# Kernel tuning notes

Hardware: AMD Instinct MI355X
Metric: run time of the kernel (lower is better)

The kernel has to match this reference:

```python
import jax, jax.numpy as jnp
import numpy as np

B, S, D = 4, 2048, 1024
P = 9            # num_paths
DM = D // 4      # bottleneck d_mid
EPS = 1e-5


def setup_inputs() -> dict:
    key = jax.random.key(0)
    ks = jax.random.split(key, 12)
    sc_in = 1.0 / np.sqrt(D)
    sc_mid = 1.0 / np.sqrt(DM)
    return {
        "x": jax.random.normal(ks[0], (B, S, D), dtype=jnp.float32),
        # neighbor mixer: per-channel 3-tap kernel over the sequence axis
        "mix_kernel": jax.random.normal(ks[1], (3, D), dtype=jnp.float32) * 0.5,
        # 9 parallel bottleneck paths: D -> D/4 -> D
        "W1": jax.random.normal(ks[2], (P, D, DM), dtype=jnp.float32) * sc_in,
        "b1": jnp.zeros((P, DM), dtype=jnp.float32),
        "W2": jax.random.normal(ks[3], (P, DM, D), dtype=jnp.float32) * sc_mid,
        "b2": jnp.zeros((P, D), dtype=jnp.float32),
        # observer: D -> D/4 -> tanh -> ... -> P scores
        "Wo1": jax.random.normal(ks[4], (D, DM), dtype=jnp.float32) * sc_in,
        "bo1": jnp.zeros((DM,), dtype=jnp.float32),
        "Wo2": jax.random.normal(ks[5], (DM, P), dtype=jnp.float32) * sc_mid,
        "bo2": jnp.zeros((P,), dtype=jnp.float32),
        # output norm affine params
        "gamma": jnp.ones((D,), dtype=jnp.float32),
        "beta": jnp.zeros((D,), dtype=jnp.float32),
    }


def _mix(x, mix_kernel):
    # eidosNeighborMixer: local 3-tap depthwise mix along sequence (non-causal)
    xp = jnp.pad(x, ((0, 0), (1, 1), (0, 0)))
    return (mix_kernel[0] * xp[:, :-2]
            + mix_kernel[1] * xp[:, 1:-1]
            + mix_kernel[2] * xp[:, 2:])


def _layernorm(h, gamma, beta):
    mu = jnp.mean(h, axis=-1, keepdims=True)
    var = jnp.var(h, axis=-1, keepdims=True)
    return (h - mu) * jax.lax.rsqrt(var + EPS) * gamma + beta


def reference(x, mix_kernel, W1, b1, W2, b2, Wo1, bo1, Wo2, bo2, gamma, beta):
    x_mixed = _mix(x, mix_kernel)                                   # [B,S,D]
    # all num_paths bottleneck transforms computed densely (as in source)
    h = jnp.einsum("bsd,pdm->bspm", x_mixed, W1) + b1               # [B,S,P,DM]
    stacked_paths = jnp.einsum("bspm,pmd->bspd", h, W2) + b2        # [B,S,P,D]
    # observer scores
    scores = jnp.tanh(x_mixed @ Wo1 + bo1) @ Wo2 + bo2              # [B,S,P]
    # eval-mode collapse: hard argmax one-hot selection
    idx = jnp.argmax(scores, axis=-1)                               # [B,S]
    weights = jax.nn.one_hot(idx, P, dtype=stacked_paths.dtype)     # [B,S,P]
    collapsed = jnp.einsum("bspd,bsp->bsd", stacked_paths, weights)  # [B,S,D]
    return _layernorm(x + collapsed, gamma, beta)
```

## Files before the change

### kernel.cpp

```cpp
#include <hip/hip_runtime.h>
#include <math.h>

#define Ss 2048
#define Dd 1024
#define Pp 9
#define DMm 256
#define Tt 8192
#define EPSf 1e-5f
#define BAND 6e-3f

typedef __attribute__((ext_vector_type(8))) __bf16 bf16x8;
typedef __attribute__((ext_vector_type(4))) float f32x4;

#define GLOBAL_AS __attribute__((address_space(1)))
#define LDS_AS __attribute__((address_space(3)))

#define MAXTILES 137

__device__ __forceinline__ unsigned short bf16rn(float f) {
  unsigned int u = __float_as_uint(f);
  unsigned int r = (u + 0x7fffu + ((u >> 16) & 1u)) >> 16;
  return (unsigned short)r;
}

__device__ __forceinline__ void gload16(const void* g, void* l) {
  __builtin_amdgcn_global_load_lds((const GLOBAL_AS unsigned int*)g,
                                   (LDS_AS unsigned int*)l, 16, 0, 0);
}

__device__ __forceinline__ int xcd_swz(int bx, int nwg) {
  const int q = nwg >> 3, r = nwg & 7;
  const int xcd = bx & 7, loc = bx >> 3;
  return (xcd < r ? xcd * (q + 1) : r * (q + 1) + (xcd - r) * q) + loc;
}

#define KSW(r, sl) (((r) << 6) + ((((sl) ^ ((r) & 7))) << 3))

__global__ __launch_bounds__(256) void k_mix2(const float* __restrict__ x,
    const float* __restrict__ mk, unsigned short* __restrict__ xh,
    int* __restrict__ counts) {
  if (blockIdx.x == 0 && threadIdx.x < 64) counts[threadIdx.x] = 0;
  const int t = xcd_swz(blockIdx.x, Tt);
  const int s = t & (Ss - 1);
  const int d = threadIdx.x << 2;
  const float* xc = x + (size_t)t * Dd + d;
  float4 vb = *(const float4*)xc;
  float4 va = make_float4(0.f, 0.f, 0.f, 0.f);
  float4 vc = make_float4(0.f, 0.f, 0.f, 0.f);
  if (s > 0)      va = *(const float4*)(xc - Dd);
  if (s < Ss - 1) vc = *(const float4*)(xc + Dd);
  const float4 k0 = *(const float4*)(mk + d);
  const float4 k1 = *(const float4*)(mk + Dd + d);
  const float4 k2 = *(const float4*)(mk + 2 * Dd + d);
  float4 o;
  o.x = k0.x * va.x + k1.x * vb.x + k2.x * vc.x;
  o.y = k0.y * va.y + k1.y * vb.y + k2.y * vc.y;
  o.z = k0.z * va.z + k1.z * vb.z + k2.z * vc.z;
  o.w = k0.w * va.w + k1.w * vb.w + k2.w * vc.w;
  ushort4 h;
  h.x = bf16rn(o.x); h.y = bf16rn(o.y); h.z = bf16rn(o.z); h.w = bf16rn(o.w);
  *(ushort4*)(xh + (size_t)t * Dd + d) = h;
}

__global__ __launch_bounds__(256) void k_cvt_all(
    const float* __restrict__ W1, const float* __restrict__ W2,
    const float* __restrict__ Wo1,
    unsigned short* __restrict__ W1t, unsigned short* __restrict__ W2t,
    unsigned short* __restrict__ Wo1t) {
  const int z = blockIdx.z;
  const float* in; unsigned short* outp; int R, C, r0, c0;
  if (z < Pp)            { in = W1;  outp = W1t;  R = Dd;  C = DMm;
                           r0 = blockIdx.x * 32; c0 = blockIdx.y * 32; }
  else if (z < 2 * Pp)   { in = W2;  outp = W2t;  R = DMm; C = Dd;
                           r0 = blockIdx.y * 32; c0 = blockIdx.x * 32; }
  else                   { in = Wo1; outp = Wo1t; R = Dd;  C = DMm;
                           r0 = blockIdx.x * 32; c0 = blockIdx.y * 32; }
  const int zi = (z < Pp) ? z : ((z < 2 * Pp) ? z - Pp : 0);
  const size_t zo = (size_t)zi * R * C;
  __shared__ float tile[32][33];
  const int tr = threadIdx.x >> 3, tc = (threadIdx.x & 7) << 2;
  float4 v = *(const float4*)(in + zo + (size_t)(r0 + tr) * C + c0 + tc);
  tile[tr][tc] = v.x; tile[tr][tc + 1] = v.y; tile[tr][tc + 2] = v.z; tile[tr][tc + 3] = v.w;
  __syncthreads();
  ushort4 h;
  h.x = bf16rn(tile[tc + 0][tr]); h.y = bf16rn(tile[tc + 1][tr]);
  h.z = bf16rn(tile[tc + 2][tr]); h.w = bf16rn(tile[tc + 3][tr]);
  *(ushort4*)(outp + zo + (size_t)(c0 + tr) * R + r0 + tc) = h;
}

template<int KTOT, int NTOT, int MODE, bool GROUPED>
__global__ __launch_bounds__(256) void k_gemm(
    const unsigned short* __restrict__ A,
    const unsigned short* __restrict__ Bt,
    const float* __restrict__ bias,
    const float* __restrict__ resid,
    float* __restrict__ outf, unsigned short* __restrict__ outh,
    const int* __restrict__ counts, const int* __restrict__ tokenlist) {
  int p = 0, ti = xcd_swz(blockIdx.x, gridDim.x), cnt = Tt;
  if (GROUPED) {
    for (p = 0; p < Pp; ++p) {
      cnt = counts[p];
      const int nt = (cnt + 63) >> 6;
      if (ti < nt) break;
      ti -= nt;
    }
    if (p == Pp) return;
  }
  const int tile0 = ti * 64;
  __shared__ int tl[64];
  __shared__ __align__(16) unsigned short As[2][64 * 64];
  __shared__ __align__(16) unsigned short Bs[2][128 * 64];
  const int tid = threadIdx.x;
  if (tid < 64) {
    const int li = tile0 + tid;
    if (GROUPED) tl[tid] = (li < cnt) ? tokenlist[p * Tt + li] : tokenlist[p * Tt];
    else         tl[tid] = li;
  }
  __syncthreads();
  const int w = tid >> 6, lane = tid & 63;
  const int fr = lane & 15, fs = lane >> 4;
  const int wr = w >> 1, wc = w & 1;
  const int n0 = blockIdx.y * 128;
  const unsigned short* Bp0 = Bt + (size_t)p * NTOT * KTOT + (size_t)n0 * KTOT;
  const unsigned short* srcA[2];
  #pragma unroll
  for (int i = 0; i < 2; ++i) {
    const int u = i * 256 + tid, r = u >> 3, sl = (u & 7) ^ (r & 7);
    srcA[i] = A + (size_t)tl[r] * KTOT + sl * 8;
  }
  const unsigned short* srcB[4];
  #pragma unroll
  for (int i = 0; i < 4; ++i) {
    const int u = i * 256 + tid, r = u >> 3, sl = (u & 7) ^ (r & 7);
    srcB[i] = Bp0 + (size_t)r * KTOT + sl * 8;
  }
  const int ldsW = w * 512;
  int aoff[2][2], boff[4][2];
  #pragma unroll
  for (int m = 0; m < 2; ++m)
    #pragma unroll
    for (int kk = 0; kk < 2; ++kk)
      aoff[m][kk] = KSW(wr * 32 + m * 16 + fr, kk * 4 + fs);
  #pragma unroll
  for (int n = 0; n < 4; ++n)
    #pragma unroll
    for (int kk = 0; kk < 2; ++kk)
      boff[n][kk] = KSW(wc * 64 + n * 16 + fr, kk * 4 + fs);

#define STAGE(b, kb) do { \
    gload16(srcA[0] + (kb), &As[b][0] + ldsW); \
    gload16(srcA[1] + (kb), &As[b][0] + 2048 + ldsW); \
    gload16(srcB[0] + (kb), &Bs[b][0] + ldsW); \
    gload16(srcB[1] + (kb), &Bs[b][0] + 2048 + ldsW); \
    gload16(srcB[2] + (kb), &Bs[b][0] + 4096 + ldsW); \
    gload16(srcB[3] + (kb), &Bs[b][0] + 6144 + ldsW); \
  } while (0)

  f32x4 acc[2][4] = {};
  const int NS = KTOT / 64;
  STAGE(0, 0);
  for (int s = 0; s < NS; ++s) {
    const int buf = s & 1;
    if (s + 1 < NS) {
      STAGE(buf ^ 1, (s + 1) * 64);
      asm volatile("s_waitcnt vmcnt(6)" ::: "memory");
    } else {
      asm volatile("s_waitcnt vmcnt(0)" ::: "memory");
    }
    __builtin_amdgcn_s_barrier();
    __builtin_amdgcn_sched_barrier(0);
    const unsigned short* Ab = &As[buf][0];
    const unsigned short* Bb_ = &Bs[buf][0];
    bf16x8 a[2][2], b[4][2];
    #pragma unroll
    for (int m = 0; m < 2; ++m)
      #pragma unroll
      for (int kk = 0; kk < 2; ++kk)
        a[m][kk] = *(const bf16x8*)&Ab[aoff[m][kk]];
    #pragma unroll
    for (int n = 0; n < 4; ++n)
      #pragma unroll
      for (int kk = 0; kk < 2; ++kk)
        b[n][kk] = *(const bf16x8*)&Bb_[boff[n][kk]];
    #pragma unroll
    for (int kk = 0; kk < 2; ++kk)
      #pragma unroll
      for (int m = 0; m < 2; ++m)
        #pragma unroll
        for (int n = 0; n < 4; ++n)
          acc[m][n] = __builtin_amdgcn_mfma_f32_16x16x32_bf16(a[m][kk], b[n][kk], acc[m][n], 0, 0, 0);
    __builtin_amdgcn_s_barrier();
  }
#undef STAGE

  const float* bias_z = bias + (size_t)p * NTOT;
  #pragma unroll
  for (int m = 0; m < 2; ++m) {
    #pragma unroll
    for (int j = 0; j < 4; ++j) {
      const int rr = wr * 32 + m * 16 + fs * 4 + j;
      const int li = tile0 + rr;
      if (GROUPED && li >= cnt) continue;
      const int t = tl[rr];
      #pragma unroll
      for (int n = 0; n < 4; ++n) {
        const int c = n0 + wc * 64 + n * 16 + fr;
        const float v = acc[m][n][j] + bias_z[c];
        if (MODE == 0)      outf[(size_t)t * NTOT + c] = tanhf(v);
        else if (MODE == 1) outh[(size_t)t * NTOT + c] = bf16rn(v);
        else                outf[(size_t)t * NTOT + c] = v + resid[(size_t)t * NTOT + c];
      }
    }
  }
}

__global__ __launch_bounds__(256) void k_score(const float* __restrict__ hidden,
    const float* __restrict__ Wo2, const float* __restrict__ bo2,
    int* __restrict__ idx, int* __restrict__ nflag, int* __restrict__ flagged) {
  __shared__ float sW[DMm * Pp];
  const int tid = threadIdx.x;
  for (int l = tid; l < DMm * Pp; l += 256) sW[l] = Wo2[l];
  __syncthreads();
  const int wave = tid >> 6, lane = tid & 63;
  const int t = blockIdx.x * 4 + wave;
  const float4 h = *(const float4*)(hidden + (size_t)t * DMm + lane * 4);
  const int m = lane * 4;
  float part[Pp];
  #pragma unroll
  for (int pp = 0; pp < Pp; ++pp)
    part[pp] = h.x * sW[(m + 0) * Pp + pp] + h.y * sW[(m + 1) * Pp + pp]
             + h.z * sW[(m + 2) * Pp + pp] + h.w * sW[(m + 3) * Pp + pp];
  #pragma unroll
  for (int off = 32; off > 0; off >>= 1)
    #pragma unroll
    for (int pp = 0; pp < Pp; ++pp)
      part[pp] += __shfl_xor(part[pp], off);
  if (lane == 0) {
    float best = -1e30f, second = -1e30f;
    int bi = 0;
    #pragma unroll
    for (int pp = 0; pp < Pp; ++pp) {
      const float sc = part[pp] + bo2[pp];
      if (sc > best) { second = best; best = sc; bi = pp; }
      else if (sc > second) second = sc;
    }
    idx[t] = bi;
    if (best - second < BAND) {
      const int pos = atomicAdd(nflag, 1);
      flagged[pos] = t;
    }
  }
}

__global__ __launch_bounds__(256) void k_rescue(const float* __restrict__ x,
    const float* __restrict__ mk,
    const float* __restrict__ Wo1, const float* __restrict__ bo1,
    const float* __restrict__ Wo2, const float* __restrict__ bo2,
    const int* __restrict__ nflag, const int* __restrict__ flagged,
    int* __restrict__ idx) {
  __shared__ double sx[Dd];
  __shared__ double th[DMm];
  __shared__ double red[4][12];
  const int nf = *nflag;
  const int tid = threadIdx.x;
  const int wv = tid >> 6, ln = tid & 63;
  for (int f = blockIdx.x; f < nf; f += gridDim.x) {
    const int t = flagged[f];
    const int s = t & (Ss - 1);
    for (int l = tid; l < Dd; l += 256) {
      const double xa = (s > 0)      ? (double)x[(size_t)(t - 1) * Dd + l] : 0.0;
      const double xb =                (double)x[(size_t)t * Dd + l];
      const double xc = (s < Ss - 1) ? (double)x[(size_t)(t + 1) * Dd + l] : 0.0;
      sx[l] = (double)mk[l] * xa + (double)mk[Dd + l] * xb + (double)mk[2 * Dd + l] * xc;
    }
    __syncthreads();
    {
      double a0 = 0, a1 = 0, a2 = 0, a3 = 0;
      const float* wcol = Wo1 + tid;
      for (int d = 0; d < Dd; d += 4) {
        a0 += sx[d + 0] * (double)wcol[(size_t)(d + 0) * DMm];
        a1 += sx[d + 1] * (double)wcol[(size_t)(d + 1) * DMm];
        a2 += sx[d + 2] * (double)wcol[(size_t)(d + 2) * DMm];
        a3 += sx[d + 3] * (double)wcol[(size_t)(d + 3) * DMm];
      }
      th[tid] = tanh(((a0 + a1) + (a2 + a3)) + (double)bo1[tid]);
    }
    __syncthreads();
    double pr[Pp];
    const double tv = th[tid];
    #pragma unroll
    for (int p = 0; p < Pp; ++p) pr[p] = tv * (double)Wo2[tid * Pp + p];
    #pragma unroll
    for (int off = 32; off > 0; off >>= 1)
      #pragma unroll
      for (int p = 0; p < Pp; ++p) pr[p] += __shfl_xor(pr[p], off);
    if (ln == 0) {
      #pragma unroll
      for (int p = 0; p < Pp; ++p) red[wv][p] = pr[p];
    }
    __syncthreads();
    if (tid == 0) {
      double best = -1e300; int bi = 0;
      #pragma unroll
      for (int p = 0; p < Pp; ++p) {
        const double sv = red[0][p] + red[1][p] + red[2][p] + red[3][p] + (double)bo2[p];
        if (sv > best) { best = sv; bi = p; }
      }
      idx[t] = bi;
    }
    __syncthreads();
  }
}

__global__ __launch_bounds__(256) void k_scatter(const int* __restrict__ idx,
    int* __restrict__ counts, int* __restrict__ tokenlist) {
  __shared__ int lcnt[Pp], lbase[Pp];
  const int tid = threadIdx.x;
  if (tid < Pp) lcnt[tid] = 0;
  __syncthreads();
  const int t = blockIdx.x * 256 + tid;
  const int p = idx[t];
  const int slot = atomicAdd(&lcnt[p], 1);
  __syncthreads();
  if (tid < Pp) lbase[tid] = atomicAdd(&counts[tid], lcnt[tid]);
  __syncthreads();
  tokenlist[p * Tt + lbase[p] + slot] = t;
}

__global__ __launch_bounds__(256) void k_ln(float* __restrict__ y,
    const float* __restrict__ gamma, const float* __restrict__ beta) {
  const int t = blockIdx.x;
  const int d = threadIdx.x << 2;
  float* row = y + (size_t)t * Dd;
  float4 v = *(float4*)(row + d);
  float s = v.x + v.y + v.z + v.w;
  float q = v.x * v.x + v.y * v.y + v.z * v.z + v.w * v.w;
  #pragma unroll
  for (int off = 32; off > 0; off >>= 1) {
    s += __shfl_xor(s, off);
    q += __shfl_xor(q, off);
  }
  __shared__ float ssum[4], sqq[4];
  const int wave = threadIdx.x >> 6, lane = threadIdx.x & 63;
  if (lane == 0) { ssum[wave] = s; sqq[wave] = q; }
  __syncthreads();
  s = ssum[0] + ssum[1] + ssum[2] + ssum[3];
  q = sqq[0] + sqq[1] + sqq[2] + sqq[3];
  const float mu = s * (1.f / Dd);
  const float var = q * (1.f / Dd) - mu * mu;
  const float inv = rsqrtf(var + EPSf);
  const float4 g = *(const float4*)(gamma + d);
  const float4 bt = *(const float4*)(beta + d);
  float4 o;
  o.x = (v.x - mu) * inv * g.x + bt.x;
  o.y = (v.y - mu) * inv * g.y + bt.y;
  o.z = (v.z - mu) * inv * g.z + bt.z;
  o.w = (v.w - mu) * inv * g.w + bt.w;
  *(float4*)(row + d) = o;
}

extern "C" void kernel_launch(void* const* d_in, const int* in_sizes, int n_in,
                              void* d_out, int out_size, void* d_ws, size_t ws_size,
                              hipStream_t stream) {
  (void)in_sizes; (void)n_in; (void)out_size; (void)ws_size;
  const float* x     = (const float*)d_in[0];
  const float* mk    = (const float*)d_in[1];
  const float* W1    = (const float*)d_in[2];
  const float* b1    = (const float*)d_in[3];
  const float* W2    = (const float*)d_in[4];
  const float* b2    = (const float*)d_in[5];
  const float* Wo1   = (const float*)d_in[6];
  const float* bo1   = (const float*)d_in[7];
  const float* Wo2   = (const float*)d_in[8];
  const float* bo2   = (const float*)d_in[9];
  const float* gamma = (const float*)d_in[10];
  const float* beta  = (const float*)d_in[11];
  float* out = (float*)d_out;

  size_t off = 0;
  auto alloc = [&](size_t bytes) -> void* {
    void* p = (char*)d_ws + off;
    off += (bytes + 255) & ~(size_t)255;
    return p;
  };
  unsigned short* xm_h   = (unsigned short*)alloc((size_t)Tt * Dd * 2);
  float*          hidden = (float*)alloc((size_t)Tt * DMm * 4);
  unsigned short* h1     = (unsigned short*)hidden;
  unsigned short* W1t    = (unsigned short*)alloc((size_t)Pp * Dd * DMm * 2);
  unsigned short* W2t    = (unsigned short*)alloc((size_t)Pp * DMm * Dd * 2);
  unsigned short* Wo1t   = (unsigned short*)alloc((size_t)Dd * DMm * 2);
  int* idx      = (int*)alloc(Tt * 4);
  int* counts   = (int*)alloc(64 * 4);
  int* nflag    = counts + 16;
  int* flagged  = (int*)alloc(Tt * 4);
  int* tokenlist = (int*)alloc((size_t)Pp * Tt * 4);

  k_mix2<<<Tt, 256, 0, stream>>>(x, mk, xm_h, counts);
  k_cvt_all<<<dim3(32, 8, 2 * Pp + 1), 256, 0, stream>>>(W1, W2, Wo1, W1t, W2t, Wo1t);

  k_gemm<Dd, DMm, 0, false><<<dim3(Tt / 64, DMm / 128), 256, 0, stream>>>(
      xm_h, Wo1t, bo1, nullptr, hidden, nullptr, nullptr, nullptr);
  k_score<<<Tt / 4, 256, 0, stream>>>(hidden, Wo2, bo2, idx, nflag, flagged);
  k_rescue<<<256, 256, 0, stream>>>(x, mk, Wo1, bo1, Wo2, bo2, nflag, flagged, idx);
  k_scatter<<<Tt / 256, 256, 0, stream>>>(idx, counts, tokenlist);

  k_gemm<Dd, DMm, 1, true><<<dim3(MAXTILES, DMm / 128), 256, 0, stream>>>(
      xm_h, W1t, b1, nullptr, nullptr, h1, counts, tokenlist);
  k_gemm<DMm, Dd, 2, true><<<dim3(MAXTILES, Dd / 128), 256, 0, stream>>>(
      h1, W2t, b2, x, out, nullptr, counts, tokenlist);
  k_ln<<<Tt, 256, 0, stream>>>(out, gamma, beta);
}
```

Before: 137.1 us.

## Merge mix and weight-convert kernels; use 32-row M tiles for narrow GEMMs

Fuses the sequence-mix/bf16 conversion kernel and the weight transpose/convert kernel into one launch, with the block index selecting the role. Templates the GEMM on M tile height and uses 32-row tiles for the two K=1024, N=256 GEMMs (observer and first path projection), doubling their block count so the GPU has more parallelism. The wait count is adjusted to match the smaller number of A loads. Smaller tiles reduce per-block reuse of the B operand and add more per-group tile rounding overhead.

Result: faster. 132.4 us (-3.4%).

```diff
diff --git a/kernel.cpp b/kernel.cpp
--- a/kernel.cpp
+++ b/kernel.cpp
@@ -16,6 +16,7 @@
 #define LDS_AS __attribute__((address_space(3)))
 
 #define MAXTILES 137
+#define MAXT32   265
 
 __device__ __forceinline__ unsigned short bf16rn(float f) {
   unsigned int u = __float_as_uint(f);
@@ -36,45 +37,44 @@
 
 #define KSW(r, sl) (((r) << 6) + ((((sl) ^ ((r) & 7))) << 3))
 
-__global__ __launch_bounds__(256) void k_mix2(const float* __restrict__ x,
+__global__ __launch_bounds__(256) void k_prep(const float* __restrict__ x,
     const float* __restrict__ mk, unsigned short* __restrict__ xh,
-    int* __restrict__ counts) {
-  if (blockIdx.x == 0 && threadIdx.x < 64) counts[threadIdx.x] = 0;
-  const int t = xcd_swz(blockIdx.x, Tt);
-  const int s = t & (Ss - 1);
-  const int d = threadIdx.x << 2;
-  const float* xc = x + (size_t)t * Dd + d;
-  float4 vb = *(const float4*)xc;
-  float4 va = make_float4(0.f, 0.f, 0.f, 0.f);
-  float4 vc = make_float4(0.f, 0.f, 0.f, 0.f);
-  if (s > 0)      va = *(const float4*)(xc - Dd);
-  if (s < Ss - 1) vc = *(const float4*)(xc + Dd);
-  const float4 k0 = *(const float4*)(mk + d);
-  const float4 k1 = *(const float4*)(mk + Dd + d);
-  const float4 k2 = *(const float4*)(mk + 2 * Dd + d);
-  float4 o;
-  o.x = k0.x * va.x + k1.x * vb.x + k2.x * vc.x;
-  o.y = k0.y * va.y + k1.y * vb.y + k2.y * vc.y;
-  o.z = k0.z * va.z + k1.z * vb.z + k2.z * vc.z;
-  o.w = k0.w * va.w + k1.w * vb.w + k2.w * vc.w;
-  ushort4 h;
-  h.x = bf16rn(o.x); h.y = bf16rn(o.y); h.z = bf16rn(o.z); h.w = bf16rn(o.w);
-  *(ushort4*)(xh + (size_t)t * Dd + d) = h;
-}
-
-__global__ __launch_bounds__(256) void k_cvt_all(
     const float* __restrict__ W1, const float* __restrict__ W2,
     const float* __restrict__ Wo1,
     unsigned short* __restrict__ W1t, unsigned short* __restrict__ W2t,
-    unsigned short* __restrict__ Wo1t) {
-  const int z = blockIdx.z;
+    unsigned short* __restrict__ Wo1t, int* __restrict__ counts) {
+  const int bid = blockIdx.x;
+  if (bid < Tt) {
+    if (bid == 0 && threadIdx.x < 64) counts[threadIdx.x] = 0;
+    const int t = xcd_swz(bid, Tt);
+    const int s = t & (Ss - 1);
+    const int d = threadIdx.x << 2;
+    const float* xc = x + (size_t)t * Dd + d;
+    float4 vb = *(const float4*)xc;
+    float4 va = make_float4(0.f, 0.f, 0.f, 0.f);
+    float4 vc = make_float4(0.f, 0.f, 0.f, 0.f);
+    if (s > 0)      va = *(const float4*)(xc - Dd);
+    if (s < Ss - 1) vc = *(const float4*)(xc + Dd);
+    const float4 k0 = *(const float4*)(mk + d);
+    const float4 k1 = *(const float4*)(mk + Dd + d);
+    const float4 k2 = *(const float4*)(mk + 2 * Dd + d);
+    float4 o;
+    o.x = k0.x * va.x + k1.x * vb.x + k2.x * vc.x;
+    o.y = k0.y * va.y + k1.y * vb.y + k2.y * vc.y;
+    o.z = k0.z * va.z + k1.z * vb.z + k2.z * vc.z;
+    o.w = k0.w * va.w + k1.w * vb.w + k2.w * vc.w;
+    ushort4 h;
+    h.x = bf16rn(o.x); h.y = bf16rn(o.y); h.z = bf16rn(o.z); h.w = bf16rn(o.w);
+    *(ushort4*)(xh + (size_t)t * Dd + d) = h;
+    return;
+  }
+  const int i = bid - Tt;
+  const int z = i >> 8, rem = i & 255;
+  const int bx = rem & 31, by = rem >> 5;
   const float* in; unsigned short* outp; int R, C, r0, c0;
-  if (z < Pp)            { in = W1;  outp = W1t;  R = Dd;  C = DMm;
-                           r0 = blockIdx.x * 32; c0 = blockIdx.y * 32; }
-  else if (z < 2 * Pp)   { in = W2;  outp = W2t;  R = DMm; C = Dd;
-                           r0 = blockIdx.y * 32; c0 = blockIdx.x * 32; }
-  else                   { in = Wo1; outp = Wo1t; R = Dd;  C = DMm;
-                           r0 = blockIdx.x * 32; c0 = blockIdx.y * 32; }
+  if (z < Pp)          { in = W1;  outp = W1t;  R = Dd;  C = DMm; r0 = bx * 32; c0 = by * 32; }
+  else if (z < 2 * Pp) { in = W2;  outp = W2t;  R = DMm; C = Dd;  r0 = by * 32; c0 = bx * 32; }
+  else                 { in = Wo1; outp = Wo1t; R = Dd;  C = DMm; r0 = bx * 32; c0 = by * 32; }
   const int zi = (z < Pp) ? z : ((z < 2 * Pp) ? z - Pp : 0);
   const size_t zo = (size_t)zi * R * C;
   __shared__ float tile[32][33];
@@ -88,7 +88,7 @@
   *(ushort4*)(outp + zo + (size_t)(c0 + tr) * R + r0 + tc) = h;
 }
 
-template<int KTOT, int NTOT, int MODE, bool GROUPED>
+template<int KTOT, int NTOT, int MODE, bool GROUPED, int TM>
 __global__ __launch_bounds__(256) void k_gemm(
     const unsigned short* __restrict__ A,
     const unsigned short* __restrict__ Bt,
@@ -96,22 +96,23 @@
     const float* __restrict__ resid,
     float* __restrict__ outf, unsigned short* __restrict__ outh,
     const int* __restrict__ counts, const int* __restrict__ tokenlist) {
+  constexpr int MM = TM / 32;
   int p = 0, ti = xcd_swz(blockIdx.x, gridDim.x), cnt = Tt;
   if (GROUPED) {
     for (p = 0; p < Pp; ++p) {
       cnt = counts[p];
-      const int nt = (cnt + 63) >> 6;
+      const int nt = (cnt + TM - 1) / TM;
       if (ti < nt) break;
       ti -= nt;
     }
     if (p == Pp) return;
   }
-  const int tile0 = ti * 64;
-  __shared__ int tl[64];
-  __shared__ __align__(16) unsigned short As[2][64 * 64];
+  const int tile0 = ti * TM;
+  __shared__ int tl[TM];
+  __shared__ __align__(16) unsigned short As[2][TM * 64];
   __shared__ __align__(16) unsigned short Bs[2][128 * 64];
   const int tid = threadIdx.x;
-  if (tid < 64) {
+  if (tid < TM) {
     const int li = tile0 + tid;
     if (GROUPED) tl[tid] = (li < cnt) ? tokenlist[p * Tt + li] : tokenlist[p * Tt];
     else         tl[tid] = li;
@@ -122,9 +123,9 @@
   const int wr = w >> 1, wc = w & 1;
   const int n0 = blockIdx.y * 128;
   const unsigned short* Bp0 = Bt + (size_t)p * NTOT * KTOT + (size_t)n0 * KTOT;
-  const unsigned short* srcA[2];
-  #pragma unroll
-  for (int i = 0; i < 2; ++i) {
+  const unsigned short* srcA[MM];
+  #pragma unroll
+  for (int i = 0; i < MM; ++i) {
     const int u = i * 256 + tid, r = u >> 3, sl = (u & 7) ^ (r & 7);
     srcA[i] = A + (size_t)tl[r] * KTOT + sl * 8;
   }
@@ -135,12 +136,12 @@
     srcB[i] = Bp0 + (size_t)r * KTOT + sl * 8;
   }
   const int ldsW = w * 512;
-  int aoff[2][2], boff[4][2];
-  #pragma unroll
-  for (int m = 0; m < 2; ++m)
+  int aoff[MM][2], boff[4][2];
+  #pragma unroll
+  for (int m = 0; m < MM; ++m)
     #pragma unroll
     for (int kk = 0; kk < 2; ++kk)
-      aoff[m][kk] = KSW(wr * 32 + m * 16 + fr, kk * 4 + fs);
+      aoff[m][kk] = KSW(wr * (TM / 2) + m * 16 + fr, kk * 4 + fs);
   #pragma unroll
   for (int n = 0; n < 4; ++n)
     #pragma unroll
@@ -148,22 +149,24 @@
       boff[n][kk] = KSW(wc * 64 + n * 16 + fr, kk * 4 + fs);
 
 #define STAGE(b, kb) do { \
-    gload16(srcA[0] + (kb), &As[b][0] + ldsW); \
-    gload16(srcA[1] + (kb), &As[b][0] + 2048 + ldsW); \
+    _Pragma("unroll") \
+    for (int i = 0; i < MM; ++i) \
+      gload16(srcA[i] + (kb), &As[b][0] + i * 2048 + ldsW); \
     gload16(srcB[0] + (kb), &Bs[b][0] + ldsW); \
     gload16(srcB[1] + (kb), &Bs[b][0] + 2048 + ldsW); \
     gload16(srcB[2] + (kb), &Bs[b][0] + 4096 + ldsW); \
     gload16(srcB[3] + (kb), &Bs[b][0] + 6144 + ldsW); \
   } while (0)
 
-  f32x4 acc[2][4] = {};
+  f32x4 acc[MM][4] = {};
   const int NS = KTOT / 64;
   STAGE(0, 0);
   for (int s = 0; s < NS; ++s) {
     const int buf = s & 1;
     if (s + 1 < NS) {
       STAGE(buf ^ 1, (s + 1) * 64);
-      asm volatile("s_waitcnt vmcnt(6)" ::: "memory");
+      if (TM == 64) asm volatile("s_waitcnt vmcnt(6)" ::: "memory");
+      else          asm volatile("s_waitcnt vmcnt(5)" ::: "memory");
     } else {
       asm volatile("s_waitcnt vmcnt(0)" ::: "memory");
     }
@@ -171,9 +174,9 @@
     __builtin_amdgcn_sched_barrier(0);
     const unsigned short* Ab = &As[buf][0];
     const unsigned short* Bb_ = &Bs[buf][0];
-    bf16x8 a[2][2], b[4][2];
-    #pragma unroll
-    for (int m = 0; m < 2; ++m)
+    bf16x8 a[MM][2], b[4][2];
+    #pragma unroll
+    for (int m = 0; m < MM; ++m)
       #pragma unroll
       for (int kk = 0; kk < 2; ++kk)
         a[m][kk] = *(const bf16x8*)&Ab[aoff[m][kk]];
@@ -185,7 +188,7 @@
     #pragma unroll
     for (int kk = 0; kk < 2; ++kk)
       #pragma unroll
-      for (int m = 0; m < 2; ++m)
+      for (int m = 0; m < MM; ++m)
         #pragma unroll
         for (int n = 0; n < 4; ++n)
           acc[m][n] = __builtin_amdgcn_mfma_f32_16x16x32_bf16(a[m][kk], b[n][kk], acc[m][n], 0, 0, 0);
@@ -195,10 +198,10 @@
 
   const float* bias_z = bias + (size_t)p * NTOT;
   #pragma unroll
-  for (int m = 0; m < 2; ++m) {
+  for (int m = 0; m < MM; ++m) {
     #pragma unroll
     for (int j = 0; j < 4; ++j) {
-      const int rr = wr * 32 + m * 16 + fs * 4 + j;
+      const int rr = wr * (TM / 2) + m * 16 + fs * 4 + j;
       const int li = tile0 + rr;
       if (GROUPED && li >= cnt) continue;
       const int t = tl[rr];
@@ -395,18 +398,18 @@
   int* flagged  = (int*)alloc(Tt * 4);
   int* tokenlist = (int*)alloc((size_t)Pp * Tt * 4);
 
-  k_mix2<<<Tt, 256, 0, stream>>>(x, mk, xm_h, counts);
-  k_cvt_all<<<dim3(32, 8, 2 * Pp + 1), 256, 0, stream>>>(W1, W2, Wo1, W1t, W2t, Wo1t);
-
-  k_gemm<Dd, DMm, 0, false><<<dim3(Tt / 64, DMm / 128), 256, 0, stream>>>(
+  k_prep<<<Tt + (2 * Pp + 1) * 256, 256, 0, stream>>>(
+      x, mk, xm_h, W1, W2, Wo1, W1t, W2t, Wo1t, counts);
+
+  k_gemm<Dd, DMm, 0, false, 32><<<dim3(Tt / 32, DMm / 128), 256, 0, stream>>>(
       xm_h, Wo1t, bo1, nullptr, hidden, nullptr, nullptr, nullptr);
   k_score<<<Tt / 4, 256, 0, stream>>>(hidden, Wo2, bo2, idx, nflag, flagged);
   k_rescue<<<256, 256, 0, stream>>>(x, mk, Wo1, bo1, Wo2, bo2, nflag, flagged, idx);
   k_scatter<<<Tt / 256, 256, 0, stream>>>(idx, counts, tokenlist);
 
-  k_gemm<Dd, DMm, 1, true><<<dim3(MAXTILES, DMm / 128), 256, 0, stream>>>(
+  k_gemm<Dd, DMm, 1, true, 32><<<dim3(MAXT32, DMm / 128), 256, 0, stream>>>(
       xm_h, W1t, b1, nullptr, nullptr, h1, counts, tokenlist);
-  k_gemm<DMm, Dd, 2, true><<<dim3(MAXTILES, Dd / 128), 256, 0, stream>>>(
+  k_gemm<DMm, Dd, 2, true, 64><<<dim3(MAXTILES, Dd / 128), 256, 0, stream>>>(
       h1, W2t, b2, x, out, nullptr, counts, tokenlist);
   k_ln<<<Tt, 256, 0, stream>>>(out, gamma, beta);
 }
```
